# Kernel optimization log

Measured on AMD Instinct MI355X. Metric: run time of the kernel, lower is better.

## Reference

```python
import jax, jax.numpy as jnp
import numpy as np

B, S, D, H = 2, 2048, 1024, 16
DEPTH = D // H
NEG = -1.0e9


def setup_inputs() -> dict:
    key = jax.random.key(0)
    ks = jax.random.split(key, 12)
    s = 1.0 / np.sqrt(D)
    return {
        "q": jax.random.normal(ks[0], (B, S, D), jnp.float32),
        "k": jax.random.normal(ks[1], (B, S, D), jnp.float32),
        "v": jax.random.normal(ks[2], (B, S, D), jnp.float32),
        "mask": jax.random.randint(ks[3], (B, 1, 1, S), 0, 2).astype(jnp.float32),
        "wq": jax.random.normal(ks[4], (D, D), jnp.float32) * s,
        "bq": jnp.zeros((D,), jnp.float32),
        "wk": jax.random.normal(ks[5], (D, D), jnp.float32) * s,
        "bk": jnp.zeros((D,), jnp.float32),
        "wv": jax.random.normal(ks[6], (D, D), jnp.float32) * s,
        "bv": jnp.zeros((D,), jnp.float32),
        "wo": jax.random.normal(ks[7], (D, D), jnp.float32) * s,
        "bo": jnp.zeros((D,), jnp.float32),
    }


def _split_heads(x):
    # [B, S, D] -> [B, H, S, depth]
    b, s, _ = x.shape
    return x.reshape(b, s, H, DEPTH).transpose(0, 2, 1, 3)


def reference(q, k, v, mask, wq, bq, wk, bk, wv, bv, wo, bo):
    qh = _split_heads(q @ wq + bq)
    kh = _split_heads(k @ wk + bk)
    vh = _split_heads(v @ wv + bv)
    scale = 1.0 / jnp.sqrt(jnp.asarray(DEPTH, jnp.float32))
    logits = jnp.einsum("bhqd,bhkd->bhqk", qh, kh) * scale
    logits = logits + mask * NEG
    attn = jax.nn.softmax(logits, axis=-1)  # [B, H, Sq, Skv]
    out = jnp.einsum("bhqk,bhkd->bhqd", attn, vh)
    out = out.transpose(0, 2, 1, 3).reshape(q.shape[0], -1, D)
    out = out @ wo + bo
    return out, attn
```

## Files before the change

### kernel.cpp

```cpp
#include <hip/hip_runtime.h>

typedef unsigned short u16;
typedef unsigned int   u32;
typedef __bf16 bf16x8 __attribute__((ext_vector_type(8)));
typedef float  f32x4  __attribute__((ext_vector_type(4)));
typedef u16    u16x8  __attribute__((ext_vector_type(8)));

#define S_   2048
#define D_   1024
#define H_   16
#define M_   4096

#define SCALE2 0.18033688011112042f
#define MASKC  (-1.4426950408889634e9f)
#define SHIFT2 11.541560327111707f

__device__ __forceinline__ u16 f2b(float f){
  union { float f; u32 i; } x; x.f = f;
  u32 u = x.i;
  u32 r = (u + 0x7fffu + ((u >> 16) & 1u)) >> 16;
  return (u16)r;
}
__device__ __forceinline__ void async16(u16* lds, const u16* g){
  __builtin_amdgcn_global_load_lds((const __attribute__((address_space(1))) void*)g,
                                   (__attribute__((address_space(3))) void*)lds, 16, 0, 0);
}
__device__ __forceinline__ f32x4 mma16(bf16x8 a, bf16x8 b, f32x4 c){
  return __builtin_amdgcn_mfma_f32_16x16x32_bf16(a, b, c, 0, 0, 0);
}
__device__ __forceinline__ bf16x8 ld_frag_u16(const u16* p){
  u16x8 v = *(const u16x8*)p;
  return __builtin_bit_cast(bf16x8, v);
}

__global__ __launch_bounds__(256) void prep(
    const float* __restrict__ q, const float* __restrict__ k, const float* __restrict__ v,
    u16* __restrict__ qb, u16* __restrict__ kb, u16* __restrict__ vb,
    const float* __restrict__ w0, const float* __restrict__ w1,
    const float* __restrict__ w2, const float* __restrict__ w3,
    u16* __restrict__ t0, u16* __restrict__ t1,
    u16* __restrict__ t2, u16* __restrict__ t3)
{
  const int bid = blockIdx.x;
  if (bid < 6144){
    const int which = bid >> 11;
    const int bx = bid & 2047;
    const float* x = (which == 0) ? q : (which == 1) ? k : v;
    u16* y = (which == 0) ? qb : (which == 1) ? kb : vb;
    size_t i = (size_t)bx * 256 + threadIdx.x;
    const f32x4* p = (const f32x4*)(x + i * 8);
    f32x4 a = p[0], b = p[1];
    u16x8 o;
    o[0] = f2b(a[0]); o[1] = f2b(a[1]); o[2] = f2b(a[2]); o[3] = f2b(a[3]);
    o[4] = f2b(b[0]); o[5] = f2b(b[1]); o[6] = f2b(b[2]); o[7] = f2b(b[3]);
    *(u16x8*)(y + i * 8) = o;
  } else {
    const int b = bid - 6144;
    const int z = b >> 8, rem = b & 255, by = rem >> 4, bx = rem & 15;
    const float* W; u16* T;
    switch (z){
      case 0: W = w0; T = t0; break;
      case 1: W = w1; T = t1; break;
      case 2: W = w2; T = t2; break;
      default: W = w3; T = t3; break;
    }
    __shared__ u16 tile[64][65];
    const int t = threadIdx.x;
    const int r0 = by * 64, c0 = bx * 64;
    const int row = t >> 2, cg = t & 3;
    const float* src = W + (size_t)(r0 + row) * D_ + c0 + cg * 16;
    f32x4 a0 = *(const f32x4*)(src + 0);
    f32x4 a1 = *(const f32x4*)(src + 4);
    f32x4 a2 = *(const f32x4*)(src + 8);
    f32x4 a3 = *(const f32x4*)(src + 12);
    #pragma unroll
    for (int e = 0; e < 4; ++e){
      tile[row][cg*16 +      e] = f2b(a0[e]);
      tile[row][cg*16 +  4 + e] = f2b(a1[e]);
      tile[row][cg*16 +  8 + e] = f2b(a2[e]);
      tile[row][cg*16 + 12 + e] = f2b(a3[e]);
    }
    __syncthreads();
    u16* dst = T + (size_t)(c0 + row) * D_ + r0 + cg * 16;
    u16x8 oa, ob;
    #pragma unroll
    for (int e = 0; e < 8; ++e){ oa[e] = tile[cg*16 + e][row]; ob[e] = tile[cg*16 + 8 + e][row]; }
    *(u16x8*)dst = oa;
    *(u16x8*)(dst + 8) = ob;
  }
}

__global__ __launch_bounds__(256) void gemm_qkv(
    const u16* __restrict__ qb, const u16* __restrict__ kb, const u16* __restrict__ vb,
    const u16* __restrict__ wqT, const u16* __restrict__ wkT, const u16* __restrict__ wvT,
    const float* __restrict__ bq, const float* __restrict__ bk, const float* __restrict__ bv,
    u16* __restrict__ Qh, u16* __restrict__ Kh, u16* __restrict__ Vt)
{
  __shared__ __attribute__((aligned(16))) u16 smem[128 * 132];
  u16* As = smem;
  u16* Bs = smem + 128 * 64;
  const u16 *A, *Bt; const float* bias; u16* Cb;
  switch (blockIdx.z){
    case 0: A = qb; Bt = wqT; bias = bq; Cb = Qh; break;
    case 1: A = kb; Bt = wkT; bias = bk; Cb = Kh; break;
    default: A = vb; Bt = wvT; bias = bv; Cb = Vt; break;
  }
  const bool vtr = (blockIdx.z == 2);
  const int tid = threadIdx.x;
  const int wave = tid >> 6, lane = tid & 63, ln = lane & 15, quad = lane >> 4;
  const int wm = wave >> 1, wn = wave & 1;
  const int m0 = blockIdx.x * 128, n0 = blockIdx.y * 128;

  f32x4 acc[4][4];
  #pragma unroll
  for (int i = 0; i < 4; ++i)
    #pragma unroll
    for (int j = 0; j < 4; ++j) acc[i][j] = (f32x4){0.f, 0.f, 0.f, 0.f};

  for (int kt = 0; kt < D_; kt += 64){
    #pragma unroll
    for (int it = 0; it < 4; ++it){
      int i = it * 256 + tid;
      int r = i >> 3, c = i & 7, cs = c ^ (r & 7);
      async16(&As[i * 8], &A [(size_t)(m0 + r) * D_ + kt + cs * 8]);
      async16(&Bs[i * 8], &Bt[(size_t)(n0 + r) * D_ + kt + cs * 8]);
    }
    __syncthreads();
    #pragma unroll
    for (int kk = 0; kk < 2; ++kk){
      bf16x8 af[4], bfr[4];
      #pragma unroll
      for (int i4 = 0; i4 < 4; ++i4){
        int row = wm * 64 + i4 * 16 + ln;
        af[i4] = ld_frag_u16(&As[row * 64 + ((kk * 4 + quad) ^ (row & 7)) * 8]);
      }
      #pragma unroll
      for (int j4 = 0; j4 < 4; ++j4){
        int row = wn * 64 + j4 * 16 + ln;
        bfr[j4] = ld_frag_u16(&Bs[row * 64 + ((kk * 4 + quad) ^ (row & 7)) * 8]);
      }
      #pragma unroll
      for (int i4 = 0; i4 < 4; ++i4)
        #pragma unroll
        for (int j4 = 0; j4 < 4; ++j4)
          acc[i4][j4] = mma16(af[i4], bfr[j4], acc[i4][j4]);
    }
    __syncthreads();
  }

  #pragma unroll
  for (int j4 = 0; j4 < 4; ++j4){
    int nl = wn * 64 + j4 * 16 + ln;
    float biasv = bias[n0 + nl];
    #pragma unroll
    for (int i4 = 0; i4 < 4; ++i4){
      #pragma unroll
      for (int rg = 0; rg < 4; ++rg){
        int ml = wm * 64 + i4 * 16 + quad * 4 + rg;
        u16 hv = f2b(acc[i4][j4][rg] + biasv);
        smem[vtr ? (nl * 132 + ml) : (ml * 132 + nl)] = hv;
      }
    }
  }
  __syncthreads();
  const int bb = m0 >> 11, sbase = m0 & 2047;
  #pragma unroll
  for (int c = 0; c < 8; ++c){
    int task = c * 256 + tid;
    int rr = task >> 4, ch = task & 15;
    u16x8 val = *(const u16x8*)&smem[rr * 132 + ch * 8];
    if (vtr){
      int hh = (n0 + rr) >> 6, dc = (n0 + rr) & 63;
      *(u16x8*)&Cb[((size_t)(bb * H_ + hh) * 64 + dc) * S_ + sbase + ch * 8] = val;
    } else {
      int s = sbase + rr;
      int nn = n0 + ch * 8, hh = nn >> 6, dc = nn & 63;
      *(u16x8*)&Cb[((size_t)(bb * H_ + hh) * S_ + s) * 64 + dc] = val;
    }
  }
}

__global__ __launch_bounds__(256) void gemm_o(
    const u16* __restrict__ A, const u16* __restrict__ Bt,
    const float* __restrict__ bias, float* __restrict__ Cf)
{
  __shared__ __attribute__((aligned(16))) u16 As[2][128 * 64];
  __shared__ __attribute__((aligned(16))) u16 Bs[2][128 * 64];
  const int tid = threadIdx.x;
  const int wave = tid >> 6, lane = tid & 63, ln = lane & 15, quad = lane >> 4;
  const int wm = wave >> 1, wn = wave & 1;
  const int m0 = blockIdx.x * 128, n0 = blockIdx.y * 128;

  f32x4 acc[4][4];
  #pragma unroll
  for (int i = 0; i < 4; ++i)
    #pragma unroll
    for (int j = 0; j < 4; ++j) acc[i][j] = (f32x4){0.f, 0.f, 0.f, 0.f};

  #pragma unroll
  for (int it = 0; it < 4; ++it){
    int i = it * 256 + tid;
    int r = i >> 3, c = i & 7, cs = c ^ (r & 7);
    async16(&As[0][i * 8], &A [(size_t)(m0 + r) * D_ + cs * 8]);
    async16(&Bs[0][i * 8], &Bt[(size_t)(n0 + r) * D_ + cs * 8]);
  }
  __syncthreads();

  int cur = 0;
  for (int kt = 0; kt < D_; kt += 64){
    if (kt + 64 < D_){
      int nb = cur ^ 1;
      #pragma unroll
      for (int it = 0; it < 4; ++it){
        int i = it * 256 + tid;
        int r = i >> 3, c = i & 7, cs = c ^ (r & 7);
        async16(&As[nb][i * 8], &A [(size_t)(m0 + r) * D_ + kt + 64 + cs * 8]);
        async16(&Bs[nb][i * 8], &Bt[(size_t)(n0 + r) * D_ + kt + 64 + cs * 8]);
      }
    }
    #pragma unroll
    for (int kk = 0; kk < 2; ++kk){
      bf16x8 af[4], bfr[4];
      #pragma unroll
      for (int i4 = 0; i4 < 4; ++i4){
        int row = wm * 64 + i4 * 16 + ln;
        af[i4] = ld_frag_u16(&As[cur][row * 64 + ((kk * 4 + quad) ^ (row & 7)) * 8]);
      }
      #pragma unroll
      for (int j4 = 0; j4 < 4; ++j4){
        int row = wn * 64 + j4 * 16 + ln;
        bfr[j4] = ld_frag_u16(&Bs[cur][row * 64 + ((kk * 4 + quad) ^ (row & 7)) * 8]);
      }
      #pragma unroll
      for (int i4 = 0; i4 < 4; ++i4)
        #pragma unroll
        for (int j4 = 0; j4 < 4; ++j4)
          acc[i4][j4] = mma16(af[i4], bfr[j4], acc[i4][j4]);
    }
    __syncthreads();
    cur ^= 1;
  }

  #pragma unroll
  for (int j4 = 0; j4 < 4; ++j4){
    int nidx = n0 + wn * 64 + j4 * 16 + ln;
    float biasv = bias[nidx];
    #pragma unroll
    for (int i4 = 0; i4 < 4; ++i4){
      #pragma unroll
      for (int rg = 0; rg < 4; ++rg){
        int r = m0 + wm * 64 + i4 * 16 + quad * 4 + rg;
        Cf[(size_t)r * D_ + nidx] = acc[i4][j4][rg] + biasv;
      }
    }
  }
}

__global__ __launch_bounds__(256) void attn_stats(
    const u16* __restrict__ Qh, const u16* __restrict__ Kh,
    const float* __restrict__ maskp, float* __restrict__ lrow)
{
  __shared__ __attribute__((aligned(16))) u16 Qs[128 * 64];
  __shared__ __attribute__((aligned(16))) u16 Ks[2][64 * 64];
  const int tid = threadIdx.x;
  const int wave = tid >> 6, lane = tid & 63, ln = lane & 15, quad = lane >> 4;
  const int orig = blockIdx.x;
  const int xcd = orig & 7, slot = orig >> 3;
  const int bh = xcd * 4 + (slot >> 4);
  const int q0 = (slot & 15) * 128;
  const int bsel = bh >> 4;

  #pragma unroll
  for (int it = 0; it < 4; ++it){
    int i = it * 256 + tid;
    int r = i >> 3, c = i & 7, cs = c ^ (r & 7);
    async16(&Qs[i * 8], &Qh[((size_t)bh * S_ + q0 + r) * 64 + cs * 8]);
  }
  #pragma unroll
  for (int it = 0; it < 2; ++it){
    int i = it * 256 + tid;
    int r = i >> 3, c = i & 7, cs = c ^ (r & 7);
    async16(&Ks[0][i * 8], &Kh[((size_t)bh * S_ + r) * 64 + cs * 8]);
  }
  __syncthreads();
  bf16x8 aq[2][2];
  #pragma unroll
  for (int f = 0; f < 2; ++f){
    int row = wave * 32 + f * 16 + ln;
    aq[f][0] = ld_frag_u16(&Qs[row * 64 + ((0 + quad) ^ (row & 7)) * 8]);
    aq[f][1] = ld_frag_u16(&Qs[row * 64 + ((4 + quad) ^ (row & 7)) * 8]);
  }

  float lsum[2][4] = {{0.f,0.f,0.f,0.f},{0.f,0.f,0.f,0.f}};
  int cur = 0;
  for (int n0 = 0; n0 < S_; n0 += 64){
    if (n0 + 64 < S_){
      int nb = cur ^ 1;
      #pragma unroll
      for (int it = 0; it < 2; ++it){
        int i = it * 256 + tid;
        int r = i >> 3, c = i & 7, cs = c ^ (r & 7);
        async16(&Ks[nb][i * 8], &Kh[((size_t)bh * S_ + n0 + 64 + r) * 64 + cs * 8]);
      }
    }
    float mv[4];
    #pragma unroll
    for (int j = 0; j < 4; ++j)
      mv[j] = maskp[bsel * S_ + n0 + j * 16 + ln] * MASKC - SHIFT2;
    #pragma unroll
    for (int j = 0; j < 4; ++j){
      int row = j * 16 + ln;
      bf16x8 b0 = ld_frag_u16(&Ks[cur][row * 64 + ((0 + quad) ^ (row & 7)) * 8]);
      bf16x8 b1 = ld_frag_u16(&Ks[cur][row * 64 + ((4 + quad) ^ (row & 7)) * 8]);
      #pragma unroll
      for (int f = 0; f < 2; ++f){
        f32x4 a = {0.f, 0.f, 0.f, 0.f};
        a = mma16(aq[f][0], b0, a);
        a = mma16(aq[f][1], b1, a);
        #pragma unroll
        for (int rg = 0; rg < 4; ++rg)
          lsum[f][rg] += exp2f(a[rg] * SCALE2 + mv[j]);
      }
    }
    __syncthreads();
    cur ^= 1;
  }
  #pragma unroll
  for (int f = 0; f < 2; ++f)
    #pragma unroll
    for (int rg = 0; rg < 4; ++rg){
      float s = lsum[f][rg];
      s += __shfl_xor(s, 1);
      s += __shfl_xor(s, 2);
      s += __shfl_xor(s, 4);
      s += __shfl_xor(s, 8);
      if (ln == 0)
        lrow[bh * S_ + q0 + wave * 32 + f * 16 + quad * 4 + rg] = s;
    }
}

__global__ __launch_bounds__(256) void attn_pv(
    const u16* __restrict__ Qh, const u16* __restrict__ Kh, const u16* __restrict__ Vt,
    const float* __restrict__ maskp, const float* __restrict__ lrow,
    float* __restrict__ attn, u16* __restrict__ OH)
{
  __shared__ __attribute__((aligned(16))) u16 Ks[2][64 * 64];
  __shared__ __attribute__((aligned(16))) u16 Vs[2][64 * 64];
  __shared__ __attribute__((aligned(16))) u16 Ps[4][32 * 72];
  const int tid = threadIdx.x;
  const int wave = tid >> 6, lane = tid & 63, ln = lane & 15, quad = lane >> 4;
  const int orig = blockIdx.x;
  const int xcd = orig & 7, slot = orig >> 3;
  const int bh = xcd * 4 + (slot >> 4);
  const int q0 = (slot & 15) * 128;
  const int bsel = bh >> 4;

  bf16x8 aq[2][2];
  #pragma unroll
  for (int f = 0; f < 2; ++f){
    const u16* qp = &Qh[((size_t)bh * S_ + q0 + wave * 32 + f * 16 + ln) * 64 + quad * 8];
    aq[f][0] = ld_frag_u16(qp);
    aq[f][1] = ld_frag_u16(qp + 32);
  }
  float il[2][4];
  #pragma unroll
  for (int f = 0; f < 2; ++f)
    #pragma unroll
    for (int rg = 0; rg < 4; ++rg){
      int row = q0 + wave * 32 + f * 16 + quad * 4 + rg;
      il[f][rg] = 1.0f / lrow[bh * S_ + row];
    }
  f32x4 oacc[2][4];
  #pragma unroll
  for (int f = 0; f < 2; ++f)
    #pragma unroll
    for (int jd = 0; jd < 4; ++jd) oacc[f][jd] = (f32x4){0.f, 0.f, 0.f, 0.f};

  #pragma unroll
  for (int it = 0; it < 2; ++it){
    int i = it * 256 + tid;
    int r = i >> 3, c = i & 7, cs = c ^ (r & 7);
    async16(&Ks[0][i * 8], &Kh[((size_t)bh * S_ + r) * 64 + cs * 8]);
    async16(&Vs[0][i * 8], &Vt[((size_t)bh * 64 + r) * S_ + cs * 8]);
  }
  __syncthreads();

  int cur = 0;
  for (int n0 = 0; n0 < S_; n0 += 64){
    if (n0 + 64 < S_){
      int nb = cur ^ 1;
      #pragma unroll
      for (int it = 0; it < 2; ++it){
        int i = it * 256 + tid;
        int r = i >> 3, c = i & 7, cs = c ^ (r & 7);
        async16(&Ks[nb][i * 8], &Kh[((size_t)bh * S_ + n0 + 64 + r) * 64 + cs * 8]);
        async16(&Vs[nb][i * 8], &Vt[((size_t)bh * 64 + r) * S_ + n0 + 64 + cs * 8]);
      }
    }
    float mv[4];
    #pragma unroll
    for (int j = 0; j < 4; ++j)
      mv[j] = maskp[bsel * S_ + n0 + j * 16 + ln] * MASKC - SHIFT2;
    #pragma unroll
    for (int j = 0; j < 4; ++j){
      int row = j * 16 + ln;
      bf16x8 b0 = ld_frag_u16(&Ks[cur][row * 64 + ((0 + quad) ^ (row & 7)) * 8]);
      bf16x8 b1 = ld_frag_u16(&Ks[cur][row * 64 + ((4 + quad) ^ (row & 7)) * 8]);
      #pragma unroll
      for (int f = 0; f < 2; ++f){
        f32x4 a = {0.f, 0.f, 0.f, 0.f};
        a = mma16(aq[f][0], b0, a);
        a = mma16(aq[f][1], b1, a);
        #pragma unroll
        for (int rg = 0; rg < 4; ++rg){
          float p = exp2f(a[rg] * SCALE2 + mv[j]) * il[f][rg];
          attn[((size_t)bh * S_ + q0 + wave * 32 + f * 16 + quad * 4 + rg) * S_ + n0 + j * 16 + ln] = p;
          Ps[wave][(f * 16 + quad * 4 + rg) * 72 + j * 16 + ln] = f2b(p);
        }
      }
    }
    #pragma unroll
    for (int f = 0; f < 2; ++f){
      #pragma unroll
      for (int kk = 0; kk < 2; ++kk){
        bf16x8 pa = ld_frag_u16(&Ps[wave][(f * 16 + ln) * 72 + kk * 32 + quad * 8]);
        #pragma unroll
        for (int jd = 0; jd < 4; ++jd){
          int row = jd * 16 + ln;
          bf16x8 vb = ld_frag_u16(&Vs[cur][row * 64 + ((kk * 4 + quad) ^ (row & 7)) * 8]);
          oacc[f][jd] = mma16(pa, vb, oacc[f][jd]);
        }
      }
    }
    __syncthreads();
    cur ^= 1;
  }
  const int b = bh >> 4, h = bh & 15;
  #pragma unroll
  for (int f = 0; f < 2; ++f)
    #pragma unroll
    for (int jd = 0; jd < 4; ++jd)
      #pragma unroll
      for (int rg = 0; rg < 4; ++rg){
        int row = q0 + wave * 32 + f * 16 + quad * 4 + rg;
        OH[((size_t)b * S_ + row) * D_ + h * 64 + jd * 16 + ln] = f2b(oacc[f][jd][rg]);
      }
}

extern "C" void kernel_launch(void* const* d_in, const int* in_sizes, int n_in,
                              void* d_out, int out_size, void* d_ws, size_t ws_size,
                              hipStream_t stream)
{
  const float* q    = (const float*)d_in[0];
  const float* k    = (const float*)d_in[1];
  const float* v    = (const float*)d_in[2];
  const float* mask = (const float*)d_in[3];
  const float* wq   = (const float*)d_in[4];
  const float* bq   = (const float*)d_in[5];
  const float* wk   = (const float*)d_in[6];
  const float* bk   = (const float*)d_in[7];
  const float* wv   = (const float*)d_in[8];
  const float* bv   = (const float*)d_in[9];
  const float* wo   = (const float*)d_in[10];
  const float* bo   = (const float*)d_in[11];

  char* ws = (char*)d_ws;
  u16* wqT = (u16*)(ws + 0ull);
  u16* wkT = (u16*)(ws + 2097152ull);
  u16* wvT = (u16*)(ws + 4194304ull);
  u16* woT = (u16*)(ws + 6291456ull);
  u16* qb  = (u16*)(ws + 8388608ull);
  u16* kb  = (u16*)(ws + 16777216ull);
  u16* vb  = (u16*)(ws + 25165824ull);
  u16* Qh  = (u16*)(ws + 33554432ull);
  u16* Kh  = (u16*)(ws + 41943040ull);
  u16* Vt  = (u16*)(ws + 50331648ull);
  u16* OH  = (u16*)(ws + 58720256ull);
  float* lrow = (float*)(ws + 67108864ull);

  float* out  = (float*)d_out;
  float* attn = out + 4194304ull;

  prep<<<dim3(7168), 256, 0, stream>>>(q, k, v, qb, kb, vb,
                                       wq, wk, wv, wo, wqT, wkT, wvT, woT);
  gemm_qkv<<<dim3(32, 8, 3), 256, 0, stream>>>(qb, kb, vb, wqT, wkT, wvT,
                                               bq, bk, bv, Qh, Kh, Vt);
  attn_stats<<<dim3(512), 256, 0, stream>>>(Qh, Kh, mask, lrow);
  attn_pv<<<dim3(512), 256, 0, stream>>>(Qh, Kh, Vt, mask, lrow, attn, OH);
  gemm_o<<<dim3(32, 8), 256, 0, stream>>>(OH, woT, bo, out);
}
```

Before: 810.5 us.

## Double-buffer QKV GEMM loads and relax attention barrier waits with nontemporal stores

The QKV projection GEMM now prefetches the next K-tile into a second LDS buffer while computing on the current one. In the attention kernel, the large attention-probability writes use nontemporal stores. The per-tile __syncthreads is replaced by a partial vmcnt wait plus s_barrier, so outstanding attn stores need not drain every iteration. The partial vmcnt count relies on a specific number of in-flight memory ops, which is fragile if the instruction mix changes.

```diff
diff --git a/kernel.cpp b/kernel.cpp
--- a/kernel.cpp
+++ b/kernel.cpp
@@ -96,9 +96,7 @@
     const float* __restrict__ bq, const float* __restrict__ bk, const float* __restrict__ bv,
     u16* __restrict__ Qh, u16* __restrict__ Kh, u16* __restrict__ Vt)
 {
-  __shared__ __attribute__((aligned(16))) u16 smem[128 * 132];
-  u16* As = smem;
-  u16* Bs = smem + 128 * 64;
+  __shared__ __attribute__((aligned(16))) u16 smem[32768];
   const u16 *A, *Bt; const float* bias; u16* Cb;
   switch (blockIdx.z){
     case 0: A = qb; Bt = wqT; bias = bq; Cb = Qh; break;
@@ -117,27 +115,42 @@
     #pragma unroll
     for (int j = 0; j < 4; ++j) acc[i][j] = (f32x4){0.f, 0.f, 0.f, 0.f};
 
+  #pragma unroll
+  for (int it = 0; it < 4; ++it){
+    int i = it * 256 + tid;
+    int r = i >> 3, c = i & 7, cs = c ^ (r & 7);
+    async16(&smem[i * 8],         &A [(size_t)(m0 + r) * D_ + cs * 8]);
+    async16(&smem[16384 + i * 8], &Bt[(size_t)(n0 + r) * D_ + cs * 8]);
+  }
+  __syncthreads();
+
+  int cur = 0;
   for (int kt = 0; kt < D_; kt += 64){
-    #pragma unroll
-    for (int it = 0; it < 4; ++it){
-      int i = it * 256 + tid;
-      int r = i >> 3, c = i & 7, cs = c ^ (r & 7);
-      async16(&As[i * 8], &A [(size_t)(m0 + r) * D_ + kt + cs * 8]);
-      async16(&Bs[i * 8], &Bt[(size_t)(n0 + r) * D_ + kt + cs * 8]);
-    }
-    __syncthreads();
+    if (kt + 64 < D_){
+      u16* An = &smem[(cur ^ 1) * 8192];
+      u16* Bn = &smem[16384 + (cur ^ 1) * 8192];
+      #pragma unroll
+      for (int it = 0; it < 4; ++it){
+        int i = it * 256 + tid;
+        int r = i >> 3, c = i & 7, cs = c ^ (r & 7);
+        async16(&An[i * 8], &A [(size_t)(m0 + r) * D_ + kt + 64 + cs * 8]);
+        async16(&Bn[i * 8], &Bt[(size_t)(n0 + r) * D_ + kt + 64 + cs * 8]);
+      }
+    }
+    const u16* Ac = &smem[cur * 8192];
+    const u16* Bc = &smem[16384 + cur * 8192];
     #pragma unroll
     for (int kk = 0; kk < 2; ++kk){
       bf16x8 af[4], bfr[4];
       #pragma unroll
       for (int i4 = 0; i4 < 4; ++i4){
         int row = wm * 64 + i4 * 16 + ln;
-        af[i4] = ld_frag_u16(&As[row * 64 + ((kk * 4 + quad) ^ (row & 7)) * 8]);
+        af[i4] = ld_frag_u16(&Ac[row * 64 + ((kk * 4 + quad) ^ (row & 7)) * 8]);
       }
       #pragma unroll
       for (int j4 = 0; j4 < 4; ++j4){
         int row = wn * 64 + j4 * 16 + ln;
-        bfr[j4] = ld_frag_u16(&Bs[row * 64 + ((kk * 4 + quad) ^ (row & 7)) * 8]);
+        bfr[j4] = ld_frag_u16(&Bc[row * 64 + ((kk * 4 + quad) ^ (row & 7)) * 8]);
       }
       #pragma unroll
       for (int i4 = 0; i4 < 4; ++i4)
@@ -146,6 +159,7 @@
           acc[i4][j4] = mma16(af[i4], bfr[j4], acc[i4][j4]);
     }
     __syncthreads();
+    cur ^= 1;
   }
 
   #pragma unroll
@@ -414,7 +428,8 @@
         #pragma unroll
         for (int rg = 0; rg < 4; ++rg){
           float p = exp2f(a[rg] * SCALE2 + mv[j]) * il[f][rg];
-          attn[((size_t)bh * S_ + q0 + wave * 32 + f * 16 + quad * 4 + rg) * S_ + n0 + j * 16 + ln] = p;
+          __builtin_nontemporal_store(
+              p, &attn[((size_t)bh * S_ + q0 + wave * 32 + f * 16 + quad * 4 + rg) * S_ + n0 + j * 16 + ln]);
           Ps[wave][(f * 16 + quad * 4 + rg) * 72 + j * 16 + ln] = f2b(p);
         }
       }
@@ -432,7 +447,11 @@
         }
       }
     }
-    __syncthreads();
+    if (n0 + 64 < S_){
+      asm volatile("s_waitcnt vmcnt(24) lgkmcnt(0)" ::: "memory");
+      __builtin_amdgcn_s_barrier();
+      __builtin_amdgcn_sched_barrier(0);
+    }
     cur ^= 1;
   }
   const int b = bh >> 4, h = bh & 15;
```

New measurement: 832.3 us. +2.7%, slower.

## Fuse softmax row-sum pass into attention PV kernel and relax loop barrier

Applied to the files above, without the earlier changes.

Merges the separate row-statistics kernel into the PV kernel: each block first sweeps K to accumulate exp sums in registers, then reuses them directly for normalization. This removes one kernel launch and the lrow global round trip, and skips the separate Q LDS staging. The per-iteration __syncthreads in the PV loop is replaced by a partial vmcnt wait plus a raw s_barrier. This lets prefetch loads stay in flight across the barrier, but it depends on correct counter accounting.

```diff
diff --git a/kernel.cpp b/kernel.cpp
--- a/kernel.cpp
+++ b/kernel.cpp
@@ -256,92 +256,9 @@
   }
 }
 
-__global__ __launch_bounds__(256) void attn_stats(
-    const u16* __restrict__ Qh, const u16* __restrict__ Kh,
-    const float* __restrict__ maskp, float* __restrict__ lrow)
-{
-  __shared__ __attribute__((aligned(16))) u16 Qs[128 * 64];
-  __shared__ __attribute__((aligned(16))) u16 Ks[2][64 * 64];
-  const int tid = threadIdx.x;
-  const int wave = tid >> 6, lane = tid & 63, ln = lane & 15, quad = lane >> 4;
-  const int orig = blockIdx.x;
-  const int xcd = orig & 7, slot = orig >> 3;
-  const int bh = xcd * 4 + (slot >> 4);
-  const int q0 = (slot & 15) * 128;
-  const int bsel = bh >> 4;
-
-  #pragma unroll
-  for (int it = 0; it < 4; ++it){
-    int i = it * 256 + tid;
-    int r = i >> 3, c = i & 7, cs = c ^ (r & 7);
-    async16(&Qs[i * 8], &Qh[((size_t)bh * S_ + q0 + r) * 64 + cs * 8]);
-  }
-  #pragma unroll
-  for (int it = 0; it < 2; ++it){
-    int i = it * 256 + tid;
-    int r = i >> 3, c = i & 7, cs = c ^ (r & 7);
-    async16(&Ks[0][i * 8], &Kh[((size_t)bh * S_ + r) * 64 + cs * 8]);
-  }
-  __syncthreads();
-  bf16x8 aq[2][2];
-  #pragma unroll
-  for (int f = 0; f < 2; ++f){
-    int row = wave * 32 + f * 16 + ln;
-    aq[f][0] = ld_frag_u16(&Qs[row * 64 + ((0 + quad) ^ (row & 7)) * 8]);
-    aq[f][1] = ld_frag_u16(&Qs[row * 64 + ((4 + quad) ^ (row & 7)) * 8]);
-  }
-
-  float lsum[2][4] = {{0.f,0.f,0.f,0.f},{0.f,0.f,0.f,0.f}};
-  int cur = 0;
-  for (int n0 = 0; n0 < S_; n0 += 64){
-    if (n0 + 64 < S_){
-      int nb = cur ^ 1;
-      #pragma unroll
-      for (int it = 0; it < 2; ++it){
-        int i = it * 256 + tid;
-        int r = i >> 3, c = i & 7, cs = c ^ (r & 7);
-        async16(&Ks[nb][i * 8], &Kh[((size_t)bh * S_ + n0 + 64 + r) * 64 + cs * 8]);
-      }
-    }
-    float mv[4];
-    #pragma unroll
-    for (int j = 0; j < 4; ++j)
-      mv[j] = maskp[bsel * S_ + n0 + j * 16 + ln] * MASKC - SHIFT2;
-    #pragma unroll
-    for (int j = 0; j < 4; ++j){
-      int row = j * 16 + ln;
-      bf16x8 b0 = ld_frag_u16(&Ks[cur][row * 64 + ((0 + quad) ^ (row & 7)) * 8]);
-      bf16x8 b1 = ld_frag_u16(&Ks[cur][row * 64 + ((4 + quad) ^ (row & 7)) * 8]);
-      #pragma unroll
-      for (int f = 0; f < 2; ++f){
-        f32x4 a = {0.f, 0.f, 0.f, 0.f};
-        a = mma16(aq[f][0], b0, a);
-        a = mma16(aq[f][1], b1, a);
-        #pragma unroll
-        for (int rg = 0; rg < 4; ++rg)
-          lsum[f][rg] += exp2f(a[rg] * SCALE2 + mv[j]);
-      }
-    }
-    __syncthreads();
-    cur ^= 1;
-  }
-  #pragma unroll
-  for (int f = 0; f < 2; ++f)
-    #pragma unroll
-    for (int rg = 0; rg < 4; ++rg){
-      float s = lsum[f][rg];
-      s += __shfl_xor(s, 1);
-      s += __shfl_xor(s, 2);
-      s += __shfl_xor(s, 4);
-      s += __shfl_xor(s, 8);
-      if (ln == 0)
-        lrow[bh * S_ + q0 + wave * 32 + f * 16 + quad * 4 + rg] = s;
-    }
-}
-
-__global__ __launch_bounds__(256) void attn_pv(
+__global__ __launch_bounds__(256) void attn_fused(
     const u16* __restrict__ Qh, const u16* __restrict__ Kh, const u16* __restrict__ Vt,
-    const float* __restrict__ maskp, const float* __restrict__ lrow,
+    const float* __restrict__ maskp,
     float* __restrict__ attn, u16* __restrict__ OH)
 {
   __shared__ __attribute__((aligned(16))) u16 Ks[2][64 * 64];
@@ -362,14 +279,62 @@
     aq[f][0] = ld_frag_u16(qp);
     aq[f][1] = ld_frag_u16(qp + 32);
   }
+
+  #pragma unroll
+  for (int it = 0; it < 2; ++it){
+    int i = it * 256 + tid;
+    int r = i >> 3, c = i & 7, cs = c ^ (r & 7);
+    async16(&Ks[0][i * 8], &Kh[((size_t)bh * S_ + r) * 64 + cs * 8]);
+  }
+  __syncthreads();
+
+  float lsum[2][4] = {{0.f,0.f,0.f,0.f},{0.f,0.f,0.f,0.f}};
+  int cur = 0;
+  for (int n0 = 0; n0 < S_; n0 += 64){
+    if (n0 + 64 < S_){
+      int nb = cur ^ 1;
+      #pragma unroll
+      for (int it = 0; it < 2; ++it){
+        int i = it * 256 + tid;
+        int r = i >> 3, c = i & 7, cs = c ^ (r & 7);
+        async16(&Ks[nb][i * 8], &Kh[((size_t)bh * S_ + n0 + 64 + r) * 64 + cs * 8]);
+      }
+    }
+    float mv[4];
+    #pragma unroll
+    for (int j = 0; j < 4; ++j)
+      mv[j] = maskp[bsel * S_ + n0 + j * 16 + ln] * MASKC - SHIFT2;
+    #pragma unroll
+    for (int j = 0; j < 4; ++j){
+      int row = j * 16 + ln;
+      bf16x8 b0 = ld_frag_u16(&Ks[cur][row * 64 + ((0 + quad) ^ (row & 7)) * 8]);
+      bf16x8 b1 = ld_frag_u16(&Ks[cur][row * 64 + ((4 + quad) ^ (row & 7)) * 8]);
+      #pragma unroll
+      for (int f = 0; f < 2; ++f){
+        f32x4 a = {0.f, 0.f, 0.f, 0.f};
+        a = mma16(aq[f][0], b0, a);
+        a = mma16(aq[f][1], b1, a);
+        #pragma unroll
+        for (int rg = 0; rg < 4; ++rg)
+          lsum[f][rg] += exp2f(a[rg] * SCALE2 + mv[j]);
+      }
+    }
+    __syncthreads();
+    cur ^= 1;
+  }
   float il[2][4];
   #pragma unroll
   for (int f = 0; f < 2; ++f)
     #pragma unroll
     for (int rg = 0; rg < 4; ++rg){
-      int row = q0 + wave * 32 + f * 16 + quad * 4 + rg;
-      il[f][rg] = 1.0f / lrow[bh * S_ + row];
-    }
+      float s = lsum[f][rg];
+      s += __shfl_xor(s, 1);
+      s += __shfl_xor(s, 2);
+      s += __shfl_xor(s, 4);
+      s += __shfl_xor(s, 8);
+      il[f][rg] = 1.0f / s;
+    }
+
   f32x4 oacc[2][4];
   #pragma unroll
   for (int f = 0; f < 2; ++f)
@@ -385,7 +350,7 @@
   }
   __syncthreads();
 
-  int cur = 0;
+  cur = 0;
   for (int n0 = 0; n0 < S_; n0 += 64){
     if (n0 + 64 < S_){
       int nb = cur ^ 1;
@@ -432,7 +397,11 @@
         }
       }
     }
-    __syncthreads();
+    if (n0 + 64 < S_){
+      asm volatile("s_waitcnt vmcnt(24) lgkmcnt(0)" ::: "memory");
+      __builtin_amdgcn_s_barrier();
+      __builtin_amdgcn_sched_barrier(0);
+    }
     cur ^= 1;
   }
   const int b = bh >> 4, h = bh & 15;
@@ -476,7 +445,6 @@
   u16* Kh  = (u16*)(ws + 41943040ull);
   u16* Vt  = (u16*)(ws + 50331648ull);
   u16* OH  = (u16*)(ws + 58720256ull);
-  float* lrow = (float*)(ws + 67108864ull);
 
   float* out  = (float*)d_out;
   float* attn = out + 4194304ull;
@@ -485,7 +453,6 @@
                                        wq, wk, wv, wo, wqT, wkT, wvT, woT);
   gemm_qkv<<<dim3(32, 8, 3), 256, 0, stream>>>(qb, kb, vb, wqT, wkT, wvT,
                                                bq, bk, bv, Qh, Kh, Vt);
-  attn_stats<<<dim3(512), 256, 0, stream>>>(Qh, Kh, mask, lrow);
-  attn_pv<<<dim3(512), 256, 0, stream>>>(Qh, Kh, Vt, mask, lrow, attn, OH);
+  attn_fused<<<dim3(512), 256, 0, stream>>>(Qh, Kh, Vt, mask, attn, OH);
   gemm_o<<<dim3(32, 8), 256, 0, stream>>>(OH, woT, bo, out);
 }
```

Result: slower. 843.8 us (+4.1%).
